# Kernel tuning notes

Measured on AMD Instinct MI355X. Metric: run time of the kernel, lower is better.

The kernel has to match this reference:

```python
import jax, jax.numpy as jnp
from jax import lax
import numpy as np

EPS = 1e-07


def _sum_pool3_same(x):
    """TF avg_pool2d(3,1,'SAME')*9: sum over 3x3 window, edge windows scaled by 9/valid_count."""
    # x: [b, h, w, q]
    window = (1, 3, 3, 1)
    strides = (1, 1, 1, 1)
    s = lax.reduce_window(x, 0.0, lax.add, window, strides, 'SAME')
    ones = jnp.ones((1, x.shape[1], x.shape[2], 1), dtype=x.dtype)
    cnt = lax.reduce_window(ones, 0.0, lax.add, window, strides, 'SAME')
    return s / cnt * 9.0


def setup_inputs() -> dict:
    key = jax.random.key(0)
    k1, k2 = jax.random.split(key)
    foreground = jax.random.normal(k1, (4, 64, 64, 256), dtype=jnp.float32)
    masks = jax.random.uniform(k2, (4, 256, 256, 1), dtype=jnp.float32)
    return {"foreground": foreground, "masks": masks}


def reference(foreground, masks):
    # foreground: [bz, h, w, nc]; first-call forward (att_scores_prev is None).
    bz, h, w, nc = foreground.shape
    # masks resized to feature resolution (stored as state in original; no effect on output)
    if masks.shape[1] != h:
        masks = jax.image.resize(masks, (bz, h, w, masks.shape[-1]), method='bilinear')

    # 1x1 dynamic conv kernels from the feature map itself: K[b, q, c], q = flattened (h*w)
    K = (foreground + EPS).reshape(bz, h * w, nc)
    norm = jnp.sqrt(jnp.sum(K * K, axis=-1, keepdims=True))  # L2 norm per output channel q
    K = K / norm

    # conv2d with 1x1 kernels == per-pixel inner product with every patch center
    scores = jnp.einsum('bijc,bqc->bijq', foreground, K)  # [bz, h, w, h*w]

    # propagate_size=3: 3x3 smoothing (avg_pool * 9, TF edge-count semantics)
    scores = _sum_pool3_same(scores)

    att = jax.nn.softmax(scores, axis=-1)  # softmax over the h*w patch axis

    # conv2d_transpose with the same 1x1 kernels == weighted sum of patch features
    out = jnp.einsum('bijq,bqc->bijc', att, K)  # [bz, h, w, nc]
    return out
```

## Files before the change

### kernel.cpp

```cpp
#include <hip/hip_runtime.h>


#define EPSV 1e-7f

typedef __bf16 bf16x8 __attribute__((ext_vector_type(8)));
typedef float f32x4 __attribute__((ext_vector_type(4)));
typedef unsigned short ushort8v __attribute__((ext_vector_type(8)));

__device__ __forceinline__ unsigned short f2bf(float f) {
    union { float f; unsigned int u; } x; x.f = f;
    unsigned int r = x.u + 0x7FFFu + ((x.u >> 16) & 1u);
    return (unsigned short)(r >> 16);
}

__device__ __forceinline__ f32x4 mfma16(bf16x8 a, bf16x8 b, f32x4 c) {
    return __builtin_amdgcn_mfma_f32_16x16x32_bf16(a, b, c, 0, 0, 0);
}

__device__ __forceinline__ void gload_lds16(const void* g, void* l) {
    __builtin_amdgcn_global_load_lds((const __attribute__((address_space(1))) void*)g,
                                     (__attribute__((address_space(3))) void*)l, 16, 0, 0);
}

__global__ __launch_bounds__(256) void prep_kv(const float* __restrict__ F,
                                               unsigned short* __restrict__ Khi,
                                               unsigned short* __restrict__ Vt2) {
    __shared__ unsigned short ldsT[256 * 74];
    const int tid = threadIdx.x;
    const int w = tid >> 6, lane = tid & 63;
    const int q0 = blockIdx.x * 64;
    const int b = blockIdx.y;
    const size_t bq = (size_t)b * 4096;

    for (int r = 0; r < 16; ++r) {
        const int qloc = w * 16 + r;
        const int q = q0 + qloc;
        const float4 f = *(const float4*)(F + ((bq + q) << 8) + lane * 4);
        float v0 = f.x + EPSV, v1 = f.y + EPSV, v2 = f.z + EPSV, v3 = f.w + EPSV;
        float ss = v0 * v0 + v1 * v1 + v2 * v2 + v3 * v3;
        #pragma unroll
        for (int m = 1; m <= 32; m <<= 1) ss += __shfl_xor(ss, m);
        const float inv = 1.0f / sqrtf(ss);
        const unsigned short k0 = f2bf(v0 * inv), k1 = f2bf(v1 * inv);
        const unsigned short k2 = f2bf(v2 * inv), k3 = f2bf(v3 * inv);
        ushort4 kk; kk.x = k0; kk.y = k1; kk.z = k2; kk.w = k3;
        *(ushort4*)(Khi + ((bq + q) << 8) + lane * 4) = kk;
        ldsT[(lane * 4 + 0) * 74 + qloc] = k0;
        ldsT[(lane * 4 + 1) * 74 + qloc] = k1;
        ldsT[(lane * 4 + 2) * 74 + qloc] = k2;
        ldsT[(lane * 4 + 3) * 74 + qloc] = k3;
    }
    __syncthreads();
    const int c = tid;
    const int c16v = c >> 4, l15c = c & 15;
    const size_t tbase = (size_t)b * 128 + (size_t)blockIdx.x * 2;
    const unsigned short* row = ldsT + c * 74;
    #pragma unroll
    for (int tsub = 0; tsub < 2; ++tsub) {
        const unsigned short* qrow = row + tsub * 32;
        #pragma unroll
        for (int g4v = 0; g4v < 4; ++g4v) {
            ushort8v frag;
            #pragma unroll
            for (int e = 0; e < 8; ++e)
                frag[e] = qrow[(g4v * 4 + (e >> 1)) + ((e & 1) << 4)];
            *(ushort8v*)((char*)Vt2 + ((tbase + tsub) << 14) + (c16v << 10) +
                         ((g4v * 16 + l15c) << 4)) = frag;
        }
    }
}

__global__ __launch_bounds__(256) void prep_g(const float* __restrict__ F,
                                              unsigned short* __restrict__ G) {
    __shared__ float vs[64 * 256];
    const int tid = threadIdx.x;
    const int i = blockIdx.x, b = blockIdx.y;
    const size_t bq = (size_t)b * 4096;
    const int i0 = i > 0 ? i - 1 : 0, i1 = i < 63 ? i + 1 : 63;
    #pragma unroll
    for (int k2 = 0; k2 < 16; ++k2) {
        const int cell = k2 * 256 + tid;
        const int j = cell >> 6, c4 = (cell & 63) << 2;
        float4 acc = {0.f, 0.f, 0.f, 0.f};
        for (int ii = i0; ii <= i1; ++ii) {
            const float4 f = *(const float4*)(F + ((bq + ii * 64 + j) << 8) + c4);
            acc.x += f.x; acc.y += f.y; acc.z += f.z; acc.w += f.w;
        }
        *(float4*)(vs + j * 256 + c4) = acc;
    }
    __syncthreads();
    const float ri = (float)(i1 - i0 + 1);
    #pragma unroll
    for (int k2 = 0; k2 < 16; ++k2) {
        const int cell = k2 * 256 + tid;
        const int j = cell >> 6, c4 = (cell & 63) << 2;
        const int j0 = j > 0 ? j - 1 : 0, j1 = j < 63 ? j + 1 : 63;
        float4 s = {0.f, 0.f, 0.f, 0.f};
        for (int jj = j0; jj <= j1; ++jj) {
            const float4 v = *(const float4*)(vs + jj * 256 + c4);
            s.x += v.x; s.y += v.y; s.z += v.z; s.w += v.w;
        }
        const float scale = 9.0f / (ri * (float)(j1 - j0 + 1));
        ushort4 gv; gv.x = f2bf(s.x * scale); gv.y = f2bf(s.y * scale);
        gv.z = f2bf(s.z * scale); gv.w = f2bf(s.w * scale);
        *(ushort4*)(G + ((bq + i * 64 + j) << 8) + c4) = gv;
    }
}

template <int ATOMIC>
__global__ __launch_bounds__(256, 2) void attn_main(
        const unsigned short* __restrict__ Khi, const unsigned short* __restrict__ Vt2,
        const unsigned short* __restrict__ G, float* __restrict__ wsl,
        float* __restrict__ dOut, float* __restrict__ wsO) {
    __shared__ unsigned short ldsK[2][32 * 256];
    __shared__ unsigned short ldsV[2][32 * 256];
    __shared__ unsigned int ldsP[4][32 * 20];
    const int tid = threadIdx.x;
    const int w = tid >> 6, lane = tid & 63;
    const int l15 = lane & 15, g4 = lane >> 4;

    const int bid = blockIdx.x;
    const int u = bid & 7, v = bid >> 3;
    const int group = u * 2 + (v >> 5);
    const int pb = v & 31;
    const int split = group >> 2, b = group & 3;

    const int pw = pb * 128 + w * 32;
    const size_t bq = (size_t)b * 4096;

    const char* KhiB = (const char*)Khi + ((bq + split * 1024) << 9);
    const char* VtB = (const char*)Vt2 + (((size_t)b * 128 + split * 32) << 14);

    #pragma unroll
    for (int it = 0; it < 4; ++it) {
        const int g = it * 256 + tid;
        const int row = g >> 5, pos = g & 31;
        gload_lds16(KhiB + row * 512 + ((pos ^ (row & 7)) << 4),
                    (char*)&ldsK[0][0] + g * 16);
    }
    #pragma unroll
    for (int it = 0; it < 4; ++it) {
        const int g = it * 256 + tid;
        gload_lds16(VtB + g * 16, (char*)&ldsV[0][0] + g * 16);
    }

    bf16x8 a[2][8];
    #pragma unroll
    for (int rt = 0; rt < 2; ++rt)
        #pragma unroll
        for (int kg = 0; kg < 8; ++kg)
            a[rt][kg] = *(const bf16x8*)(G + ((bq + pw + rt * 16 + l15) << 8) + (kg << 5) + (g4 << 3));

    f32x4 o[2][16];
    float lacc[2][4];
    #pragma unroll
    for (int rt = 0; rt < 2; ++rt) {
        #pragma unroll
        for (int c16 = 0; c16 < 16; ++c16) o[rt][c16] = f32x4{0.f, 0.f, 0.f, 0.f};
        #pragma unroll
        for (int r = 0; r < 4; ++r) lacc[rt][r] = 0.f;
    }
    unsigned int* Pw = &ldsP[w][0];

    __syncthreads();

    #pragma unroll 1
    for (int t = 0; t < 32; ++t) {
        const int cur = t & 1;

        if (t < 31) {
            const char* ks = KhiB + (size_t)(t + 1) * 16384;
            #pragma unroll
            for (int it = 0; it < 4; ++it) {
                const int g = it * 256 + tid;
                const int row = g >> 5, pos = g & 31;
                gload_lds16(ks + row * 512 + ((pos ^ (row & 7)) << 4),
                            (char*)&ldsK[cur ^ 1][0] + g * 16);
            }
            const char* vs2 = VtB + ((size_t)(t + 1) << 14);
            #pragma unroll
            for (int it = 0; it < 4; ++it) {
                const int g = it * 256 + tid;
                gload_lds16(vs2 + g * 16, (char*)&ldsV[cur ^ 1][0] + g * 16);
            }
        }

        f32x4 s[2][2];
        #pragma unroll
        for (int rt = 0; rt < 2; ++rt) {
            s[rt][0] = f32x4{0.f, 0.f, 0.f, 0.f};
            s[rt][1] = f32x4{0.f, 0.f, 0.f, 0.f};
        }
        __builtin_amdgcn_s_setprio(1);
        #pragma unroll
        for (int kg = 0; kg < 8; ++kg) {
            #pragma unroll
            for (int ct = 0; ct < 2; ++ct) {
                const int qr = ct * 16 + l15;
                const bf16x8 bk = *(const bf16x8*)((const char*)&ldsK[cur][0] + (qr << 9) +
                                    ((((kg << 2) + g4)) ^ (qr & 7)) * 16);
                s[0][ct] = mfma16(a[0][kg], bk, s[0][ct]);
                s[1][ct] = mfma16(a[1][kg], bk, s[1][ct]);
            }
        }
        __builtin_amdgcn_s_setprio(0);

        #pragma unroll
        for (int rt = 0; rt < 2; ++rt)
            #pragma unroll
            for (int r = 0; r < 4; ++r) {
                const float e0 = __expf(s[rt][0][r]);
                const float e1 = __expf(s[rt][1][r]);
                lacc[rt][r] += e0 + e1;
                Pw[(rt * 16 + g4 * 4 + r) * 20 + l15] =
                    (unsigned int)f2bf(e0) | ((unsigned int)f2bf(e1) << 16);
            }

        bf16x8 a2[2];
        a2[0] = *(const bf16x8*)((const char*)Pw + l15 * 80 + (g4 << 4));
        a2[1] = *(const bf16x8*)((const char*)Pw + (16 + l15) * 80 + (g4 << 4));
        const char* vbase = (const char*)&ldsV[cur][0] + ((g4 * 16 + l15) << 4);
        __builtin_amdgcn_s_setprio(1);
        #pragma unroll
        for (int c16 = 0; c16 < 16; ++c16) {
            const bf16x8 bv = *(const bf16x8*)(vbase + c16 * 1024);
            o[0][c16] = mfma16(bv, a2[0], o[0][c16]);
            o[1][c16] = mfma16(bv, a2[1], o[1][c16]);
        }
        __builtin_amdgcn_s_setprio(0);

        if (t < 31) __syncthreads();
    }

    #pragma unroll
    for (int rt = 0; rt < 2; ++rt)
        #pragma unroll
        for (int r = 0; r < 4; ++r) {
            float vsum = lacc[rt][r];
            #pragma unroll
            for (int m = 1; m <= 8; m <<= 1) vsum += __shfl_xor(vsum, m);
            lacc[rt][r] = vsum;
        }
    if (l15 == 0) {
        #pragma unroll
        for (int rt = 0; rt < 2; ++rt)
            #pragma unroll
            for (int r = 0; r < 4; ++r)
                wsl[(size_t)split * 16384 + bq + pw + rt * 16 + g4 * 4 + r] = lacc[rt][r];
    }

    if (!ATOMIC) {
        float* dst = (split == 0) ? dOut : (wsO + (size_t)(split - 1) * 4194304);
        #pragma unroll
        for (int rt = 0; rt < 2; ++rt)
            #pragma unroll
            for (int c16 = 0; c16 < 16; ++c16)
                *(f32x4*)(dst + ((bq + pw + rt * 16 + l15) << 8) + c16 * 16 + (g4 << 2)) = o[rt][c16];
    } else {
        #pragma unroll
        for (int rt = 0; rt < 2; ++rt)
            #pragma unroll
            for (int c16 = 0; c16 < 16; ++c16)
                #pragma unroll
                for (int r = 0; r < 4; ++r) {
                    const size_t idx = ((bq + pw + rt * 16 + l15) << 8) + c16 * 16 + (g4 << 2) + r;
                    atomicAdd(&dOut[idx], o[rt][c16][r]);
                }
    }
}

__global__ __launch_bounds__(256) void reduce_fin(float* __restrict__ dOut,
                                                  const float* __restrict__ wsO,
                                                  const float* __restrict__ wsl) {
    const int i4 = blockIdx.x * 256 + threadIdx.x;
    const int row = i4 >> 6;
    const float l = wsl[row] + wsl[16384 + row] + wsl[32768 + row] + wsl[49152 + row];
    const float inv = 1.0f / l;
    float4 v = ((const float4*)dOut)[i4];
    const float4 a = ((const float4*)wsO)[i4];
    const float4 b = ((const float4*)(wsO + 4194304))[i4];
    const float4 c = ((const float4*)(wsO + 8388608))[i4];
    v.x = (v.x + a.x + b.x + c.x) * inv;
    v.y = (v.y + a.y + b.y + c.y) * inv;
    v.z = (v.z + a.z + b.z + c.z) * inv;
    v.w = (v.w + a.w + b.w + c.w) * inv;
    ((float4*)dOut)[i4] = v;
}

__global__ __launch_bounds__(256) void divide_fin(float* __restrict__ dOut,
                                                  const float* __restrict__ wsl) {
    const int i4 = blockIdx.x * 256 + threadIdx.x;
    const int row = i4 >> 6;
    const float l = wsl[row] + wsl[16384 + row] + wsl[32768 + row] + wsl[49152 + row];
    const float inv = 1.0f / l;
    float4 v = ((const float4*)dOut)[i4];
    v.x *= inv; v.y *= inv; v.z *= inv; v.w *= inv;
    ((float4*)dOut)[i4] = v;
}

extern "C" void kernel_launch(void* const* d_in, const int* in_sizes, int n_in,
                              void* d_out, int out_size, void* d_ws, size_t ws_size,
                              hipStream_t stream) {
    const float* F = (const float*)d_in[0];
    float* out = (float*)d_out;
    char* ws = (char*)d_ws;

    unsigned short* Khi = (unsigned short*)ws;
    unsigned short* Vt2 = Khi + 4194304;
    unsigned short* G = Vt2 + 4194304;
    float* wsl = (float*)(ws + 25165824);
    float* wsO = (float*)(ws + 25165824 + 262144);
    const size_t needA = 25165824u + 262144u + 3u * 16777216u;

    prep_kv<<<dim3(64, 4), 256, 0, stream>>>(F, Khi, Vt2);
    prep_g<<<dim3(64, 4), 256, 0, stream>>>(F, G);

    if (ws_size >= needA) {
        attn_main<0><<<dim3(512), 256, 0, stream>>>(Khi, Vt2, G, wsl, out, wsO);
        reduce_fin<<<4096, 256, 0, stream>>>(out, wsO, wsl);
    } else {
        hipMemsetAsync(out, 0, 16777216, stream);
        attn_main<1><<<dim3(512), 256, 0, stream>>>(Khi, Vt2, G, wsl, out, nullptr);
        divide_fin<<<4096, 256, 0, stream>>>(out, wsl);
    }
}
```

Baseline: 138.2 us.

## Pre-swizzle K into MFMA fragment order and use native bf16 conversion

The prep kernel now stages normalized K rows in shared memory and writes them to global memory already arranged in per-lane MFMA fragment order, matching the existing V layout. The attention kernel can then load K tiles with linear global-to-LDS copies and read each fragment at lane*16 with a fixed stride, dropping the XOR swizzle address arithmetic. The exp-to-bf16 packing uses the compiler's native __bf16 conversion instead of manual rounding, and the P fragment loads are interleaved with the packing. Risks are LDS bank conflicts on the linear fragment reads, plus extra shared memory and work in the prep kernel.

```diff
diff --git a/kernel.cpp b/kernel.cpp
--- a/kernel.cpp
+++ b/kernel.cpp
@@ -23,9 +23,10 @@
 }
 
 __global__ __launch_bounds__(256) void prep_kv(const float* __restrict__ F,
-                                               unsigned short* __restrict__ Khi,
+                                               unsigned short* __restrict__ Khi2,
                                                unsigned short* __restrict__ Vt2) {
     __shared__ unsigned short ldsT[256 * 74];
+    __shared__ unsigned short ldsR[64 * 264];
     const int tid = threadIdx.x;
     const int w = tid >> 6, lane = tid & 63;
     const int q0 = blockIdx.x * 64;
@@ -44,16 +45,33 @@
         const unsigned short k0 = f2bf(v0 * inv), k1 = f2bf(v1 * inv);
         const unsigned short k2 = f2bf(v2 * inv), k3 = f2bf(v3 * inv);
         ushort4 kk; kk.x = k0; kk.y = k1; kk.z = k2; kk.w = k3;
-        *(ushort4*)(Khi + ((bq + q) << 8) + lane * 4) = kk;
+        *(ushort4*)(ldsR + qloc * 264 + lane * 4) = kk;
         ldsT[(lane * 4 + 0) * 74 + qloc] = k0;
         ldsT[(lane * 4 + 1) * 74 + qloc] = k1;
         ldsT[(lane * 4 + 2) * 74 + qloc] = k2;
         ldsT[(lane * 4 + 3) * 74 + qloc] = k3;
     }
     __syncthreads();
+
+    const size_t tbase = (size_t)b * 128 + (size_t)blockIdx.x * 2;
+
+    #pragma unroll
+    for (int tsub = 0; tsub < 2; ++tsub) {
+        char* dstK = (char*)Khi2 + ((tbase + tsub) << 14);
+        #pragma unroll
+        for (int i = 0; i < 4; ++i) {
+            const int fi = i * 256 + tid;
+            const int chunk = fi >> 6, L = fi & 63;
+            const int l15 = L & 15, g4v = L >> 4;
+            const int kg = chunk >> 1, ct = chunk & 1;
+            const int qloc = tsub * 32 + ct * 16 + l15;
+            const int c0 = kg * 32 + g4v * 8;
+            *(ushort8v*)(dstK + fi * 16) = *(const ushort8v*)(ldsR + qloc * 264 + c0);
+        }
+    }
+
     const int c = tid;
     const int c16v = c >> 4, l15c = c & 15;
-    const size_t tbase = (size_t)b * 128 + (size_t)blockIdx.x * 2;
     const unsigned short* row = ldsT + c * 74;
     #pragma unroll
     for (int tsub = 0; tsub < 2; ++tsub) {
@@ -109,7 +127,7 @@
 
 template <int ATOMIC>
 __global__ __launch_bounds__(256, 2) void attn_main(
-        const unsigned short* __restrict__ Khi, const unsigned short* __restrict__ Vt2,
+        const unsigned short* __restrict__ Khi2, const unsigned short* __restrict__ Vt2,
         const unsigned short* __restrict__ G, float* __restrict__ wsl,
         float* __restrict__ dOut, float* __restrict__ wsO) {
     __shared__ unsigned short ldsK[2][32 * 256];
@@ -128,15 +146,13 @@
     const int pw = pb * 128 + w * 32;
     const size_t bq = (size_t)b * 4096;
 
-    const char* KhiB = (const char*)Khi + ((bq + split * 1024) << 9);
+    const char* KhiB = (const char*)Khi2 + (((size_t)b * 128 + split * 32) << 14);
     const char* VtB = (const char*)Vt2 + (((size_t)b * 128 + split * 32) << 14);
 
     #pragma unroll
     for (int it = 0; it < 4; ++it) {
         const int g = it * 256 + tid;
-        const int row = g >> 5, pos = g & 31;
-        gload_lds16(KhiB + row * 512 + ((pos ^ (row & 7)) << 4),
-                    (char*)&ldsK[0][0] + g * 16);
+        gload_lds16(KhiB + g * 16, (char*)&ldsK[0][0] + g * 16);
     }
     #pragma unroll
     for (int it = 0; it < 4; ++it) {
@@ -169,13 +185,11 @@
         const int cur = t & 1;
 
         if (t < 31) {
-            const char* ks = KhiB + (size_t)(t + 1) * 16384;
+            const char* ks = KhiB + ((size_t)(t + 1) << 14);
             #pragma unroll
             for (int it = 0; it < 4; ++it) {
                 const int g = it * 256 + tid;
-                const int row = g >> 5, pos = g & 31;
-                gload_lds16(ks + row * 512 + ((pos ^ (row & 7)) << 4),
-                            (char*)&ldsK[cur ^ 1][0] + g * 16);
+                gload_lds16(ks + g * 16, (char*)&ldsK[cur ^ 1][0] + g * 16);
             }
             const char* vs2 = VtB + ((size_t)(t + 1) << 14);
             #pragma unroll
@@ -191,35 +205,35 @@
             s[rt][0] = f32x4{0.f, 0.f, 0.f, 0.f};
             s[rt][1] = f32x4{0.f, 0.f, 0.f, 0.f};
         }
+        const char* kb = (const char*)&ldsK[cur][0] + (lane << 4);
         __builtin_amdgcn_s_setprio(1);
         #pragma unroll
         for (int kg = 0; kg < 8; ++kg) {
             #pragma unroll
             for (int ct = 0; ct < 2; ++ct) {
-                const int qr = ct * 16 + l15;
-                const bf16x8 bk = *(const bf16x8*)((const char*)&ldsK[cur][0] + (qr << 9) +
-                                    ((((kg << 2) + g4)) ^ (qr & 7)) * 16);
+                const bf16x8 bk = *(const bf16x8*)(kb + (kg * 2 + ct) * 1024);
                 s[0][ct] = mfma16(a[0][kg], bk, s[0][ct]);
                 s[1][ct] = mfma16(a[1][kg], bk, s[1][ct]);
             }
         }
         __builtin_amdgcn_s_setprio(0);
 
-        #pragma unroll
-        for (int rt = 0; rt < 2; ++rt)
+        bf16x8 a2[2];
+        #pragma unroll
+        for (int rt = 0; rt < 2; ++rt) {
             #pragma unroll
             for (int r = 0; r < 4; ++r) {
                 const float e0 = __expf(s[rt][0][r]);
                 const float e1 = __expf(s[rt][1][r]);
                 lacc[rt][r] += e0 + e1;
-                Pw[(rt * 16 + g4 * 4 + r) * 20 + l15] =
-                    (unsigned int)f2bf(e0) | ((unsigned int)f2bf(e1) << 16);
+                union { __bf16 h[2]; unsigned int u; } pk;
+                pk.h[0] = (__bf16)e0; pk.h[1] = (__bf16)e1;
+                Pw[(rt * 16 + g4 * 4 + r) * 20 + l15] = pk.u;
             }
-
-        bf16x8 a2[2];
-        a2[0] = *(const bf16x8*)((const char*)Pw + l15 * 80 + (g4 << 4));
-        a2[1] = *(const bf16x8*)((const char*)Pw + (16 + l15) * 80 + (g4 << 4));
-        const char* vbase = (const char*)&ldsV[cur][0] + ((g4 * 16 + l15) << 4);
+            a2[rt] = *(const bf16x8*)((const char*)Pw + (rt * 16 + l15) * 80 + (g4 << 4));
+        }
+
+        const char* vbase = (const char*)&ldsV[cur][0] + (lane << 4);
         __builtin_amdgcn_s_setprio(1);
         #pragma unroll
         for (int c16 = 0; c16 < 16; ++c16) {
@@ -305,22 +319,22 @@
     float* out = (float*)d_out;
     char* ws = (char*)d_ws;
 
-    unsigned short* Khi = (unsigned short*)ws;
-    unsigned short* Vt2 = Khi + 4194304;
+    unsigned short* Khi2 = (unsigned short*)ws;
+    unsigned short* Vt2 = Khi2 + 4194304;
     unsigned short* G = Vt2 + 4194304;
     float* wsl = (float*)(ws + 25165824);
     float* wsO = (float*)(ws + 25165824 + 262144);
     const size_t needA = 25165824u + 262144u + 3u * 16777216u;
 
-    prep_kv<<<dim3(64, 4), 256, 0, stream>>>(F, Khi, Vt2);
+    prep_kv<<<dim3(64, 4), 256, 0, stream>>>(F, Khi2, Vt2);
     prep_g<<<dim3(64, 4), 256, 0, stream>>>(F, G);
 
     if (ws_size >= needA) {
-        attn_main<0><<<dim3(512), 256, 0, stream>>>(Khi, Vt2, G, wsl, out, wsO);
+        attn_main<0><<<dim3(512), 256, 0, stream>>>(Khi2, Vt2, G, wsl, out, wsO);
         reduce_fin<<<4096, 256, 0, stream>>>(out, wsO, wsl);
     } else {
         hipMemsetAsync(out, 0, 16777216, stream);
-        attn_main<1><<<dim3(512), 256, 0, stream>>>(Khi, Vt2, G, wsl, out, nullptr);
+        attn_main<1><<<dim3(512), 256, 0, stream>>>(Khi2, Vt2, G, wsl, out, nullptr);
         divide_fin<<<4096, 256, 0, stream>>>(out, wsl);
     }
 }
```

New measurement: 126.0 us. 8.8% less time.
